# Performance work log

Hardware: AMD Instinct MI355X
Metric: run time of the kernel (lower is better)

Reference implementation:

```python
import jax, jax.numpy as jnp
import numpy as np

HEADS = 16
DIM_HEAD = 64
SCALE = 8.0
NUM_NULL_KV = 2
NON_CAUSAL_PREFIX = 64
LN_EPS = 1e-5

def _l2norm(t):
    # F.normalize: t / max(||t||_2, eps)
    n = jnp.sqrt(jnp.sum(t * t, axis=-1, keepdims=True))
    return t / jnp.maximum(n, 1e-12)

def _layer_norm(x, gamma):
    mu = jnp.mean(x, axis=-1, keepdims=True)
    var = jnp.mean((x - mu) ** 2, axis=-1, keepdims=True)
    return (x - mu) * jax.lax.rsqrt(var + LN_EPS) * gamma  # beta buffer is zeros

def setup_inputs() -> dict:
    key = jax.random.key(0)
    ks = jax.random.split(key, 6)
    b, n, dim = 2, 2048, 1024
    inner = HEADS * DIM_HEAD
    return {
        "x": jax.random.normal(ks[0], (b, n, dim), jnp.float32),
        "gamma": jnp.ones((dim,), jnp.float32),
        "Wq": jax.random.normal(ks[1], (dim, inner), jnp.float32) * (dim ** -0.5),
        "Wkv": jax.random.normal(ks[2], (dim, 2 * DIM_HEAD), jnp.float32) * (dim ** -0.5),
        "q_scale": jnp.ones((DIM_HEAD,), jnp.float32),
        "k_scale": jnp.ones((DIM_HEAD,), jnp.float32),
        "null_kv": jax.random.normal(ks[3], (2, NUM_NULL_KV, DIM_HEAD), jnp.float32),
        "Wout": jax.random.normal(ks[4], (inner, dim), jnp.float32) * (inner ** -0.5),
    }

def reference(x, gamma, Wq, Wkv, q_scale, k_scale, null_kv, Wout):
    b, n, dim = x.shape
    # NOTE: in the torch module, kv_input = x BEFORE self.norm is applied
    kv = jnp.einsum('bnd,de->bne', x, Wkv)          # [b, n, 2*dh]
    k, v = kv[..., :DIM_HEAD], kv[..., DIM_HEAD:]    # single shared kv head (MQA)
    xn = _layer_norm(x, gamma)
    q = jnp.einsum('bnd,de->bne', xn, Wq)            # [b, n, h*dh]
    # null kv prepended
    null_k = jnp.broadcast_to(null_kv[0], (b, NUM_NULL_KV, DIM_HEAD))
    null_v = jnp.broadcast_to(null_kv[1], (b, NUM_NULL_KV, DIM_HEAD))
    k = jnp.concatenate([null_k, k], axis=1)         # [b, j, dh]
    v = jnp.concatenate([null_v, v], axis=1)
    q = q.reshape(b, n, HEADS, DIM_HEAD).transpose(0, 2, 1, 3)  # [b, h, n, dh]
    q = _l2norm(q) * q_scale
    k = _l2norm(k) * k_scale
    sim = jnp.einsum('bhid,bjd->bhij', q, k) * SCALE  # [b, h, i, j]
    i, j = n, k.shape[1]
    rows = jnp.arange(i)[:, None]
    cols = jnp.arange(j)[None, :]
    causal_mask = cols > rows + (j - i)               # triu(j - i + 1)
    prefix_free = (rows < NON_CAUSAL_PREFIX) & (cols < NON_CAUSAL_PREFIX + (j - i))
    causal_mask = causal_mask & (~prefix_free)
    neg = -jnp.finfo(sim.dtype).max
    sim = jnp.where(causal_mask, neg, sim)
    attn = jax.nn.softmax(sim, axis=-1)
    out = jnp.einsum('bhij,bjd->bhid', attn, v)       # [b, h, n, dh]
    out = out.transpose(0, 2, 1, 3).reshape(b, n, HEADS * DIM_HEAD)
    return jnp.einsum('bne,ed->bnd', out, Wout)
```

## Files before the change

kernel.cpp:

```cpp
#include <hip/hip_runtime.h>

typedef _Float16 h16;
typedef _Float16 f16x8 __attribute__((ext_vector_type(8)));
typedef _Float16 f16x4 __attribute__((ext_vector_type(4)));
typedef float f32x4 __attribute__((ext_vector_type(4)));

#define KSCALE_FOLD 11.541560327111707f

#if __has_builtin(__builtin_amdgcn_exp2f)
#define EXP2(x) __builtin_amdgcn_exp2f(x)
#else
static __device__ __forceinline__ float EXP2(float x) {
    float r; asm("v_exp_f32 %0, %1" : "=v"(r) : "v"(x)); return r;
}
#endif

__global__ __launch_bounds__(256) void pre_k(const float* __restrict__ Wq,
    const float* __restrict__ Wkv, const float* __restrict__ Wout,
    const float* __restrict__ gamma, const float* __restrict__ x,
    const float* __restrict__ nkv, const float* __restrict__ kscale,
    h16* __restrict__ W1t, h16* __restrict__ Wot, float* __restrict__ cqp,
    float* __restrict__ mu, float* __restrict__ rr, h16* __restrict__ xh,
    h16* __restrict__ Kh, h16* __restrict__ Vth)
{
    __shared__ float ts[64][65];
    int pid = blockIdx.x;
    int tid = threadIdx.x;
    if (pid < 544) {
        int bx = pid & 15, by = pid >> 4;
        int c = tid & 63, rc = tid >> 6;
        const float* src; int ld, scol, drow0; h16* dst; bool useg = false;
        if (by < 16)      { src = Wq;   ld = 1024; scol = by*64;       dst = W1t; drow0 = scol;        useg = true; }
        else if (by < 18) { src = Wkv;  ld = 128;  scol = (by-16)*64;  dst = W1t; drow0 = 1024 + scol; }
        else              { src = Wout; ld = 1024; scol = (by-18)*64;  dst = Wot; drow0 = scol; }
        float part = 0.f;
#pragma unroll
        for (int i = 0; i < 16; ++i) {
            int r = rc*16 + i;
            float v = src[(size_t)(bx*64 + r)*ld + scol + c];
            if (useg) v *= gamma[bx*64 + r];
            part += v;
            ts[r][c] = v;
        }
        if (useg) {
        }
        __syncthreads();
        if (useg) {
        }
#pragma unroll
        for (int i = 0; i < 16; ++i) {
            int r = rc*16 + i;
            dst[(size_t)(drow0 + r)*1024 + bx*64 + c] = (h16)ts[c][r];
        }
        if (useg) {
            __syncthreads();
            ts[rc][c] = part;
            __syncthreads();
            if (rc == 0) {
                float s = ts[0][c] + ts[1][c] + ts[2][c] + ts[3][c];
                cqp[(size_t)bx*1024 + scol + c] = s;
            }
        }
    } else if (pid < 1568) {
        int w = tid >> 6, l = tid & 63;
        int row = (pid - 544)*4 + w;
        const float* xr = x + (size_t)row*1024;
        float s = 0.f, ss = 0.f;
        float4 v[4];
#pragma unroll
        for (int i = 0; i < 4; ++i) {
            v[i] = *(const float4*)(xr + i*256 + l*4);
            s  += v[i].x + v[i].y + v[i].z + v[i].w;
            ss += v[i].x*v[i].x + v[i].y*v[i].y + v[i].z*v[i].z + v[i].w*v[i].w;
        }
#pragma unroll
        for (int m = 1; m < 64; m <<= 1) { s += __shfl_xor(s, m); ss += __shfl_xor(ss, m); }
        float m_ = s * (1.f/1024.f);
        float var = ss * (1.f/1024.f) - m_*m_;
        float r_ = rsqrtf(var + 1e-5f);
        if (l == 0) { mu[row] = m_; rr[row] = r_; }
        h16* xo = xh + (size_t)row*1024;
#pragma unroll
        for (int i = 0; i < 4; ++i) {
            f16x4 hv = { (h16)v[i].x, (h16)v[i].y, (h16)v[i].z, (h16)v[i].w };
            *(f16x4*)(xo + i*256 + l*4) = hv;
        }
    } else {
        int nb = pid - 1568;
        if (nb == 0 && tid < 128) {
            int t = tid >> 6, d = tid & 63;
            float kv = nkv[(0*2 + t)*64 + d];
            float ss = kv*kv;
#pragma unroll
            for (int m = 1; m < 64; m <<= 1) ss += __shfl_xor(ss, m);
            float inv = 1.f / fmaxf(sqrtf(ss), 1e-12f);
            h16 kvh = (h16)(kv * inv * kscale[d] * KSCALE_FOLD);
            Kh[(size_t)(0*2112 + t)*64 + d] = kvh;
            Kh[(size_t)(1*2112 + t)*64 + d] = kvh;
            float nv = nkv[(2 + t)*64 + d];
            Vth[(size_t)(0*64 + d)*2112 + t] = (h16)nv;
            Vth[(size_t)(1*64 + d)*2112 + t] = (h16)nv;
        }
        for (int idx = nb*256 + tid; idx < 2*62*64; idx += 2048) {
            int b = idx / (62*64), rem = idx % (62*64);
            int j = 2050 + rem/64, d = rem & 63;
            Kh[((size_t)b*2112 + j)*64 + d] = (h16)0.f;
            Vth[((size_t)b*64 + d)*2112 + j] = (h16)0.f;
        }
    }
}

template<int MODE>
__global__ __launch_bounds__(256) void gemm_k(
    const h16* __restrict__ A, const h16* __restrict__ B,
    const float* __restrict__ mu, const float* __restrict__ rr, const float* __restrict__ cqp,
    const float* __restrict__ qscale, const float* __restrict__ kscale,
    h16* __restrict__ Qh, h16* __restrict__ Kh, h16* __restrict__ Vth, float* __restrict__ outp)
{
    __shared__ h16 As[2][128*64];
    __shared__ h16 Bs[2][64*64];
    int tid = threadIdx.x;
    int w = tid >> 6, l = tid & 63;
    int lq = l & 15, qq = l >> 4;
    int arow0 = blockIdx.y*128, bcol0 = blockIdx.x*64;
    const int K = 1024;
    f32x4 acc[2][4] = {};

    auto STAGE = [&](int buf, int kt) {
#pragma unroll
        for (int i = 0; i < 4; ++i) {
            int s = i*256 + tid;
            int row = s >> 3;
            int cb = ((s & 7)*16) ^ ((row & 7) << 4);
            const char* asrc = (const char*)(A + (size_t)(arow0 + row)*K + kt) + cb;
            __builtin_amdgcn_global_load_lds(
                (const __attribute__((address_space(1))) unsigned int*)asrc,
                (__attribute__((address_space(3))) unsigned int*)((char*)&As[buf][0] + s*16), 16, 0, 0);
        }
#pragma unroll
        for (int i = 0; i < 2; ++i) {
            int s = i*256 + tid;
            int row = s >> 3;
            int cb = ((s & 7)*16) ^ ((row & 7) << 4);
            const char* bsrc = (const char*)(B + (size_t)(bcol0 + row)*K + kt) + cb;
            __builtin_amdgcn_global_load_lds(
                (const __attribute__((address_space(1))) unsigned int*)bsrc,
                (__attribute__((address_space(3))) unsigned int*)((char*)&Bs[buf][0] + s*16), 16, 0, 0);
        }
    };

    STAGE(0, 0);
    int cur = 0;
    for (int kt = 0; kt < K; kt += 64) {
        int nkt = (kt + 64 < K) ? kt + 64 : kt;
        STAGE(cur ^ 1, nkt);
        asm volatile("s_waitcnt vmcnt(6)" ::: "memory");
        __builtin_amdgcn_s_barrier();
        __builtin_amdgcn_sched_barrier(0);
        const char* Ab = (const char*)&As[cur][0];
        const char* Bb = (const char*)&Bs[cur][0];
#pragma unroll
        for (int kc = 0; kc < 2; ++kc) {
            int cb = (kc*64 + qq*16) ^ ((lq & 7) << 4);
            f16x8 af[2], bf[4];
#pragma unroll
            for (int mt = 0; mt < 2; ++mt)
                af[mt] = *(const f16x8*)(Ab + (w*32 + mt*16 + lq)*128 + cb);
#pragma unroll
            for (int nt = 0; nt < 4; ++nt)
                bf[nt] = *(const f16x8*)(Bb + (nt*16 + lq)*128 + cb);
#pragma unroll
            for (int mt = 0; mt < 2; ++mt)
#pragma unroll
                for (int nt = 0; nt < 4; ++nt)
                    acc[mt][nt] = __builtin_amdgcn_mfma_f32_16x16x32_f16(af[mt], bf[nt], acc[mt][nt], 0, 0, 0);
        }
        __builtin_amdgcn_sched_barrier(0);
        __builtin_amdgcn_s_barrier();
        cur ^= 1;
    }
    asm volatile("s_waitcnt vmcnt(0)" ::: "memory");

    int wrow0 = arow0 + w*32;
    int bx = blockIdx.x;
    if (MODE == 1) {
#pragma unroll
        for (int mt = 0; mt < 2; ++mt)
#pragma unroll
            for (int nt = 0; nt < 4; ++nt)
#pragma unroll
                for (int i = 0; i < 4; ++i)
                    outp[(size_t)(wrow0 + mt*16 + qq*4 + i)*1024 + bcol0 + nt*16 + lq] = acc[mt][nt][i];
        return;
    }
    if (bx < 16) {
        float cqv[4], qs[4];
#pragma unroll
        for (int nt = 0; nt < 4; ++nt) {
            int col = bcol0 + nt*16 + lq;
            float s = 0.f;
#pragma unroll
            for (int j = 0; j < 16; ++j) s += cqp[(size_t)j*1024 + col];
            cqv[nt] = s;
            qs[nt] = qscale[nt*16 + lq];
        }
#pragma unroll
        for (int mt = 0; mt < 2; ++mt) {
            float muv[4], rv[4], ssq[4], qv[4][4];
#pragma unroll
            for (int i = 0; i < 4; ++i) {
                int row = wrow0 + mt*16 + qq*4 + i;
                muv[i] = mu[row]; rv[i] = rr[row]; ssq[i] = 0.f;
            }
#pragma unroll
            for (int nt = 0; nt < 4; ++nt)
#pragma unroll
                for (int i = 0; i < 4; ++i) {
                    float q = rv[i]*(acc[mt][nt][i] - muv[i]*cqv[nt]);
                    qv[nt][i] = q; ssq[i] += q*q;
                }
#pragma unroll
            for (int i = 0; i < 4; ++i) {
                float s2 = ssq[i];
                s2 += __shfl_xor(s2, 1); s2 += __shfl_xor(s2, 2);
                s2 += __shfl_xor(s2, 4); s2 += __shfl_xor(s2, 8);
                ssq[i] = 1.f / fmaxf(sqrtf(s2), 1e-12f);
            }
#pragma unroll
            for (int nt = 0; nt < 4; ++nt)
#pragma unroll
                for (int i = 0; i < 4; ++i) {
                    int row = wrow0 + mt*16 + qq*4 + i;
                    Qh[(size_t)row*1024 + bcol0 + nt*16 + lq] = (h16)(qv[nt][i]*ssq[i]*qs[nt]);
                }
        }
    } else if (bx == 16) {
        float ks[4];
#pragma unroll
        for (int nt = 0; nt < 4; ++nt) ks[nt] = kscale[nt*16 + lq] * KSCALE_FOLD;
#pragma unroll
        for (int mt = 0; mt < 2; ++mt) {
            float ssq[4] = {0.f, 0.f, 0.f, 0.f};
#pragma unroll
            for (int nt = 0; nt < 4; ++nt)
#pragma unroll
                for (int i = 0; i < 4; ++i) ssq[i] += acc[mt][nt][i]*acc[mt][nt][i];
#pragma unroll
            for (int i = 0; i < 4; ++i) {
                float s2 = ssq[i];
                s2 += __shfl_xor(s2, 1); s2 += __shfl_xor(s2, 2);
                s2 += __shfl_xor(s2, 4); s2 += __shfl_xor(s2, 8);
                ssq[i] = 1.f / fmaxf(sqrtf(s2), 1e-12f);
            }
#pragma unroll
            for (int nt = 0; nt < 4; ++nt)
#pragma unroll
                for (int i = 0; i < 4; ++i) {
                    int row = wrow0 + mt*16 + qq*4 + i;
                    int b = row >> 11, ii = row & 2047;
                    Kh[((size_t)b*2112 + 2 + ii)*64 + nt*16 + lq] = (h16)(acc[mt][nt][i]*ssq[i]*ks[nt]);
                }
        }
    } else {
#pragma unroll
        for (int mt = 0; mt < 2; ++mt)
#pragma unroll
            for (int nt = 0; nt < 4; ++nt)
#pragma unroll
                for (int i = 0; i < 4; ++i) {
                    int row = wrow0 + mt*16 + qq*4 + i;
                    int b = row >> 11, ii = row & 2047;
                    Vth[((size_t)b*64 + nt*16 + lq)*2112 + 2 + ii] = (h16)acc[mt][nt][i];
                }
    }
}

__global__ __launch_bounds__(256, 4) void attn_k(const h16* __restrict__ Qh,
    const h16* __restrict__ Kh, const h16* __restrict__ Vth, h16* __restrict__ Oh)
{
    __shared__ h16 KVs[2][2][64*64];
    __shared__ h16 Ps[4][16*64];
    int id = blockIdx.x;
    int u = id >> 5;
    int qt = (u < 16) ? u : 47 - u;
    int bh = id & 31;
    int b = bh >> 4, h = bh & 15;
    int tid = threadIdx.x, w = tid >> 6, l = tid & 63;
    int lq = l & 15, qq = l >> 4;
    int qstart = qt * 64;
    int q0w = qstart + w * 16;
    h16* P = &Ps[w][0];
    int xs = (lq & 7) << 4;

    f16x8 qf[2];
#pragma unroll
    for (int kc = 0; kc < 2; ++kc)
        qf[kc] = *(const f16x8*)(Qh + (size_t)(b*2048 + q0w + lq)*1024 + h*64 + kc*32 + qq*8);

    f16x8 ones;
#pragma unroll
    for (int i = 0; i < 8; ++i) ones[i] = (h16)1.f;

    int qrow = q0w + lq;
    int thr = (qrow < 64) ? 65 : qrow + 2;

    int cbs = ((tid & 7)*16) ^ (((tid >> 3) & 7) << 4);
    const char* ksrc = (const char*)(Kh + (size_t)b*2112*64) + (size_t)(tid >> 3)*128 + cbs;
    const char* vsrc = (const char*)(Vth + (size_t)b*64*2112) + (size_t)(tid >> 3)*4224 + cbs;

    f32x4 oacc[4] = {};
    f32x4 sacc = {};

    int lastc = qstart + 65;
    if (lastc > 2049) lastc = 2049;
    int ntile = lastc/64 + 1;

    auto STAGE = [&](int buf, int kv0) {
        const char* ks = ksrc + (size_t)kv0 * 128;
        const char* vs = vsrc + (size_t)kv0 * 2;
        __builtin_amdgcn_global_load_lds((const __attribute__((address_space(1))) unsigned int*)ks,
            (__attribute__((address_space(3))) unsigned int*)(&KVs[buf][0][(w*8)*64]), 16, 0, 0);
        __builtin_amdgcn_global_load_lds((const __attribute__((address_space(1))) unsigned int*)(ks + 32*128),
            (__attribute__((address_space(3))) unsigned int*)(&KVs[buf][0][(32 + w*8)*64]), 16, 0, 0);
        __builtin_amdgcn_global_load_lds((const __attribute__((address_space(1))) unsigned int*)vs,
            (__attribute__((address_space(3))) unsigned int*)(&KVs[buf][1][(w*8)*64]), 16, 0, 0);
        __builtin_amdgcn_global_load_lds((const __attribute__((address_space(1))) unsigned int*)(vs + (size_t)32*4224),
            (__attribute__((address_space(3))) unsigned int*)(&KVs[buf][1][(32 + w*8)*64]), 16, 0, 0);
    };

    STAGE(0, 0);
    int cur = 0;
    for (int t = 0; t < ntile; ++t) {
        int kv0 = t*64;
        int nxt = (t + 1 < ntile) ? t + 1 : t;
        STAGE(cur ^ 1, nxt*64);
        asm volatile("s_waitcnt vmcnt(4)" ::: "memory");
        __builtin_amdgcn_s_barrier();
        __builtin_amdgcn_sched_barrier(0);

        bool active = (kv0 <= q0w + 17) || (q0w < 64 && kv0 < 66);
        if (active) {
            const char* Kl = (const char*)&KVs[cur][0][0];
            const char* Vl = (const char*)&KVs[cur][1][0];
            f32x4 s[4] = {};
#pragma unroll
            for (int kc = 0; kc < 2; ++kc) {
                int ko = (kc*64 + qq*16) ^ xs;
                f16x8 kf[4];
#pragma unroll
                for (int mt = 0; mt < 4; ++mt)
                    kf[mt] = *(const f16x8*)(Kl + (mt*16 + lq)*128 + ko);
#pragma unroll
                for (int mt = 0; mt < 4; ++mt)
                    s[mt] = __builtin_amdgcn_mfma_f32_16x16x32_f16(kf[mt], qf[kc], s[mt], 0, 0, 0);
            }
            if (kv0 + 63 > q0w + 2) {
#pragma unroll
                for (int mt = 0; mt < 4; ++mt)
#pragma unroll
                    for (int i = 0; i < 4; ++i) {
                        int kv = kv0 + mt*16 + qq*4 + i;
                        if (kv > thr) s[mt][i] = -__builtin_inff();
                    }
            }
#pragma unroll
            for (int mt = 0; mt < 4; ++mt)
#pragma unroll
                for (int i = 0; i < 4; ++i)
                    s[mt][i] = EXP2(s[mt][i]);
#pragma unroll
            for (int mt = 0; mt < 4; ++mt) {
                uint2 pk;
                pk.x = __builtin_bit_cast(unsigned int, __builtin_amdgcn_cvt_pkrtz(s[mt][0], s[mt][1]));
                pk.y = __builtin_bit_cast(unsigned int, __builtin_amdgcn_cvt_pkrtz(s[mt][2], s[mt][3]));
                *(uint2*)((char*)P + lq*128 + ((mt*32 + qq*8) ^ xs)) = pk;
            }
#pragma unroll
            for (int kc = 0; kc < 2; ++kc) {
                int ko = (kc*64 + qq*16) ^ xs;
                f16x8 pf = *(const f16x8*)((const char*)P + lq*128 + ko);
#pragma unroll
                for (int dm = 0; dm < 4; ++dm) {
                    f16x8 vf = *(const f16x8*)(Vl + (dm*16 + lq)*128 + ko);
                    oacc[dm] = __builtin_amdgcn_mfma_f32_16x16x32_f16(vf, pf, oacc[dm], 0, 0, 0);
                }
                sacc = __builtin_amdgcn_mfma_f32_16x16x32_f16(ones, pf, sacc, 0, 0, 0);
            }
        }
        __builtin_amdgcn_sched_barrier(0);
        __builtin_amdgcn_s_barrier();
        cur ^= 1;
    }
    asm volatile("s_waitcnt vmcnt(0)" ::: "memory");

    float inv = 1.f / sacc[0];
#pragma unroll
    for (int dm = 0; dm < 4; ++dm) {
        f16x4 ov;
#pragma unroll
        for (int i = 0; i < 4; ++i) ov[i] = (h16)(oacc[dm][i]*inv);
        *(f16x4*)(Oh + (size_t)(b*2048 + q0w + lq)*1024 + h*64 + dm*16 + qq*4) = ov;
    }
}

extern "C" void kernel_launch(void* const* d_in, const int* in_sizes, int n_in,
                              void* d_out, int out_size, void* d_ws, size_t ws_size,
                              hipStream_t stream)
{
    const float* x      = (const float*)d_in[0];
    const float* gamma  = (const float*)d_in[1];
    const float* Wq     = (const float*)d_in[2];
    const float* Wkv    = (const float*)d_in[3];
    const float* qscale = (const float*)d_in[4];
    const float* kscale = (const float*)d_in[5];
    const float* nkv    = (const float*)d_in[6];
    const float* Wout   = (const float*)d_in[7];
    float* out = (float*)d_out;
    char* ws = (char*)d_ws;

    h16* xh    = (h16*)(ws);
    h16* Qh    = (h16*)(ws + 8388608);
    h16* Oh    = (h16*)(ws + 16777216);
    h16* W1t   = (h16*)(ws + 25165824);
    h16* Wot   = (h16*)(ws + 27525120);
    h16* Kh    = (h16*)(ws + 29622272);
    h16* Vth   = (h16*)(ws + 30162944);
    float* cqp = (float*)(ws + 30703616);
    float* mu  = (float*)(ws + 30769152);
    float* rr  = (float*)(ws + 30785536);

    pre_k<<<dim3(1576), 256, 0, stream>>>(Wq, Wkv, Wout, gamma, x, nkv, kscale,
                                          W1t, Wot, cqp, mu, rr, xh, Kh, Vth);
    gemm_k<0><<<dim3(18, 32), 256, 0, stream>>>(xh, W1t, mu, rr, cqp, qscale, kscale, Qh, Kh, Vth, out);
    attn_k<<<dim3(1024), 256, 0, stream>>>(Qh, Kh, Vth, Oh);
    gemm_k<1><<<dim3(16, 32), 256, 0, stream>>>(Oh, Wot, mu, rr, cqp, qscale, kscale, Qh, Kh, Vth, out);
}
```

Measured before the change: 86.09 us.

## Double attention query tile per block to reuse K/V fragments across two row groups

The attention kernel now handles 128 query rows per block, 32 per wave, so each K and V fragment loaded from LDS feeds two MFMA column groups. Shared K/V staging is amortised over twice as many queries, and the grid halves to 512 blocks. In exchange it needs more registers (launch bounds lowered to 3 waves per SIMD), a larger P buffer, and has fewer blocks for load balancing across CUs. It also does more masked work on the causal diagonal.

Result: slower. 92.08 us (+7.0%).

```diff
diff --git a/kernel.cpp b/kernel.cpp
--- a/kernel.cpp
+++ b/kernel.cpp
@@ -42,11 +42,7 @@
             part += v;
             ts[r][c] = v;
         }
-        if (useg) {
-        }
         __syncthreads();
-        if (useg) {
-        }
 #pragma unroll
         for (int i = 0; i < 16; ++i) {
             int r = rc*16 + i;
@@ -275,43 +271,49 @@
     }
 }
 
-__global__ __launch_bounds__(256, 4) void attn_k(const h16* __restrict__ Qh,
+__global__ __launch_bounds__(256, 3) void attn_k(const h16* __restrict__ Qh,
     const h16* __restrict__ Kh, const h16* __restrict__ Vth, h16* __restrict__ Oh)
 {
     __shared__ h16 KVs[2][2][64*64];
-    __shared__ h16 Ps[4][16*64];
+    __shared__ h16 Ps[4][32*64];
     int id = blockIdx.x;
     int u = id >> 5;
-    int qt = (u < 16) ? u : 47 - u;
+    int qt = (u < 8) ? u : 23 - u;
     int bh = id & 31;
     int b = bh >> 4, h = bh & 15;
     int tid = threadIdx.x, w = tid >> 6, l = tid & 63;
     int lq = l & 15, qq = l >> 4;
-    int qstart = qt * 64;
-    int q0w = qstart + w * 16;
+    int qstart = qt * 128;
+    int q0w = qstart + w * 32;
     h16* P = &Ps[w][0];
     int xs = (lq & 7) << 4;
 
-    f16x8 qf[2];
-#pragma unroll
-    for (int kc = 0; kc < 2; ++kc)
-        qf[kc] = *(const f16x8*)(Qh + (size_t)(b*2048 + q0w + lq)*1024 + h*64 + kc*32 + qq*8);
+    f16x8 qf[2][2];
+#pragma unroll
+    for (int nt = 0; nt < 2; ++nt)
+#pragma unroll
+        for (int kc = 0; kc < 2; ++kc)
+            qf[nt][kc] = *(const f16x8*)(Qh + (size_t)(b*2048 + q0w + nt*16 + lq)*1024 + h*64 + kc*32 + qq*8);
 
     f16x8 ones;
 #pragma unroll
     for (int i = 0; i < 8; ++i) ones[i] = (h16)1.f;
 
-    int qrow = q0w + lq;
-    int thr = (qrow < 64) ? 65 : qrow + 2;
+    int thr[2];
+#pragma unroll
+    for (int nt = 0; nt < 2; ++nt) {
+        int qrow = q0w + nt*16 + lq;
+        thr[nt] = (qrow < 64) ? 65 : qrow + 2;
+    }
 
     int cbs = ((tid & 7)*16) ^ (((tid >> 3) & 7) << 4);
     const char* ksrc = (const char*)(Kh + (size_t)b*2112*64) + (size_t)(tid >> 3)*128 + cbs;
     const char* vsrc = (const char*)(Vth + (size_t)b*64*2112) + (size_t)(tid >> 3)*4224 + cbs;
 
-    f32x4 oacc[4] = {};
-    f32x4 sacc = {};
-
-    int lastc = qstart + 65;
+    f32x4 oacc[4][2] = {};
+    f32x4 sacc[2] = {};
+
+    int lastc = qstart + 129;
     if (lastc > 2049) lastc = 2049;
     int ntile = lastc/64 + 1;
 
@@ -338,11 +340,11 @@
         __builtin_amdgcn_s_barrier();
         __builtin_amdgcn_sched_barrier(0);
 
-        bool active = (kv0 <= q0w + 17) || (q0w < 64 && kv0 < 66);
+        bool active = (kv0 <= q0w + 33) || (q0w < 64 && kv0 < 66);
         if (active) {
             const char* Kl = (const char*)&KVs[cur][0][0];
             const char* Vl = (const char*)&KVs[cur][1][0];
-            f32x4 s[4] = {};
+            f32x4 s[4][2] = {};
 #pragma unroll
             for (int kc = 0; kc < 2; ++kc) {
                 int ko = (kc*64 + qq*16) ^ xs;
@@ -352,39 +354,52 @@
                     kf[mt] = *(const f16x8*)(Kl + (mt*16 + lq)*128 + ko);
 #pragma unroll
                 for (int mt = 0; mt < 4; ++mt)
-                    s[mt] = __builtin_amdgcn_mfma_f32_16x16x32_f16(kf[mt], qf[kc], s[mt], 0, 0, 0);
+#pragma unroll
+                    for (int nt = 0; nt < 2; ++nt)
+                        s[mt][nt] = __builtin_amdgcn_mfma_f32_16x16x32_f16(kf[mt], qf[nt][kc], s[mt][nt], 0, 0, 0);
             }
             if (kv0 + 63 > q0w + 2) {
 #pragma unroll
                 for (int mt = 0; mt < 4; ++mt)
 #pragma unroll
-                    for (int i = 0; i < 4; ++i) {
-                        int kv = kv0 + mt*16 + qq*4 + i;
-                        if (kv > thr) s[mt][i] = -__builtin_inff();
-                    }
+                    for (int nt = 0; nt < 2; ++nt)
+#pragma unroll
+                        for (int i = 0; i < 4; ++i) {
+                            int kv = kv0 + mt*16 + qq*4 + i;
+                            if (kv > thr[nt]) s[mt][nt][i] = -__builtin_inff();
+                        }
             }
 #pragma unroll
             for (int mt = 0; mt < 4; ++mt)
 #pragma unroll
-                for (int i = 0; i < 4; ++i)
-                    s[mt][i] = EXP2(s[mt][i]);
-#pragma unroll
-            for (int mt = 0; mt < 4; ++mt) {
-                uint2 pk;
-                pk.x = __builtin_bit_cast(unsigned int, __builtin_amdgcn_cvt_pkrtz(s[mt][0], s[mt][1]));
-                pk.y = __builtin_bit_cast(unsigned int, __builtin_amdgcn_cvt_pkrtz(s[mt][2], s[mt][3]));
-                *(uint2*)((char*)P + lq*128 + ((mt*32 + qq*8) ^ xs)) = pk;
-            }
+                for (int nt = 0; nt < 2; ++nt)
+#pragma unroll
+                    for (int i = 0; i < 4; ++i)
+                        s[mt][nt][i] = EXP2(s[mt][nt][i]);
+#pragma unroll
+            for (int nt = 0; nt < 2; ++nt)
+#pragma unroll
+                for (int mt = 0; mt < 4; ++mt) {
+                    uint2 pk;
+                    pk.x = __builtin_bit_cast(unsigned int, __builtin_amdgcn_cvt_pkrtz(s[mt][nt][0], s[mt][nt][1]));
+                    pk.y = __builtin_bit_cast(unsigned int, __builtin_amdgcn_cvt_pkrtz(s[mt][nt][2], s[mt][nt][3]));
+                    *(uint2*)((char*)P + (nt*16 + lq)*128 + ((mt*32 + qq*8) ^ xs)) = pk;
+                }
 #pragma unroll
             for (int kc = 0; kc < 2; ++kc) {
                 int ko = (kc*64 + qq*16) ^ xs;
-                f16x8 pf = *(const f16x8*)((const char*)P + lq*128 + ko);
-#pragma unroll
-                for (int dm = 0; dm < 4; ++dm) {
-                    f16x8 vf = *(const f16x8*)(Vl + (dm*16 + lq)*128 + ko);
-                    oacc[dm] = __builtin_amdgcn_mfma_f32_16x16x32_f16(vf, pf, oacc[dm], 0, 0, 0);
-                }
-                sacc = __builtin_amdgcn_mfma_f32_16x16x32_f16(ones, pf, sacc, 0, 0, 0);
+                f16x8 vf[4];
+#pragma unroll
+                for (int dm = 0; dm < 4; ++dm)
+                    vf[dm] = *(const f16x8*)(Vl + (dm*16 + lq)*128 + ko);
+#pragma unroll
+                for (int nt = 0; nt < 2; ++nt) {
+                    f16x8 pf = *(const f16x8*)((const char*)P + (nt*16 + lq)*128 + ko);
+#pragma unroll
+                    for (int dm = 0; dm < 4; ++dm)
+                        oacc[dm][nt] = __builtin_amdgcn_mfma_f32_16x16x32_f16(vf[dm], pf, oacc[dm][nt], 0, 0, 0);
+                    sacc[nt] = __builtin_amdgcn_mfma_f32_16x16x32_f16(ones, pf, sacc[nt], 0, 0, 0);
+                }
             }
         }
         __builtin_amdgcn_sched_barrier(0);
@@ -393,13 +408,16 @@
     }
     asm volatile("s_waitcnt vmcnt(0)" ::: "memory");
 
-    float inv = 1.f / sacc[0];
-#pragma unroll
-    for (int dm = 0; dm < 4; ++dm) {
-        f16x4 ov;
-#pragma unroll
-        for (int i = 0; i < 4; ++i) ov[i] = (h16)(oacc[dm][i]*inv);
-        *(f16x4*)(Oh + (size_t)(b*2048 + q0w + lq)*1024 + h*64 + dm*16 + qq*4) = ov;
+#pragma unroll
+    for (int nt = 0; nt < 2; ++nt) {
+        float inv = 1.f / sacc[nt][0];
+#pragma unroll
+        for (int dm = 0; dm < 4; ++dm) {
+            f16x4 ov;
+#pragma unroll
+            for (int i = 0; i < 4; ++i) ov[i] = (h16)(oacc[dm][nt][i]*inv);
+            *(f16x4*)(Oh + (size_t)(b*2048 + q0w + nt*16 + lq)*1024 + h*64 + dm*16 + qq*4) = ov;
+        }
     }
 }
 
@@ -432,6 +450,6 @@
     pre_k<<<dim3(1576), 256, 0, stream>>>(Wq, Wkv, Wout, gamma, x, nkv, kscale,
                                           W1t, Wot, cqp, mu, rr, xh, Kh, Vth);
     gemm_k<0><<<dim3(18, 32), 256, 0, stream>>>(xh, W1t, mu, rr, cqp, qscale, kscale, Qh, Kh, Vth, out);
-    attn_k<<<dim3(1024), 256, 0, stream>>>(Qh, Kh, Vth, Oh);
+    attn_k<<<dim3(512), 256, 0, stream>>>(Qh, Kh, Vth, Oh);
     gemm_k<1><<<dim3(16, 32), 256, 0, stream>>>(Oh, Wot, mu, rr, cqp, qscale, kscale, Qh, Kh, Vth, out);
 }
```
